# Kernel optimization log

Measured on AMD Instinct MI355X. Metric: run time of the kernel, lower is better.

The kernel has to match this reference:

```python
import jax, jax.numpy as jnp
import numpy as np

B = 512
V = 6890   # SMPL vertices
NJ = 24    # joints (global)
NB = 10    # shape betas
NP = 207   # pose blendshape features = 23*9
NJO = 19   # cocoplus output joints
PARENTS = np.array([0,0,0,0,1,2,3,4,5,6,7,8,9,9,9,12,13,14,16,17,18,19,20,21], dtype=np.int32)


def setup_inputs() -> dict:
    key = jax.random.key(0)
    ks = jax.random.split(key, 7)
    inputs = jax.random.normal(ks[0], (B, 82), jnp.float32) * 0.2  # [pose(72) | shape(10)]
    v_template = jax.random.normal(ks[1], (V, 3), jnp.float32)
    shapes = jax.random.normal(ks[2], (NB, V * 3), jnp.float32) * 0.01
    posedirs = jax.random.normal(ks[3], (NP, V * 3), jnp.float32) * 0.01
    jr = jax.random.uniform(ks[4], (V, NJ), jnp.float32)
    smpl_regressor = jr / jnp.sum(jr, axis=0, keepdims=True)          # columns sum to 1 over vertices
    w = jax.random.uniform(ks[5], (V, NJ), jnp.float32) ** 4
    lbs_weights = w / jnp.sum(w, axis=1, keepdims=True)               # rows sum to 1 over joints
    cr = jax.random.uniform(ks[6], (V, NJO), jnp.float32)
    joint_regressor = cr / jnp.sum(cr, axis=0, keepdims=True)
    parents = jnp.asarray(PARENTS)
    return {"inputs": inputs, "v_template": v_template, "shapes": shapes,
            "posedirs": posedirs, "smpl_regressor": smpl_regressor,
            "lbs_weights": lbs_weights, "joint_regressor": joint_regressor,
            "parents": parents}


def _rodrigues(pose):  # [B,72] -> [B,24,3,3]
    r = pose.reshape(-1, 3)
    angle = jnp.linalg.norm(r + 1e-8, axis=1, keepdims=True)  # [N,1]
    n = r / angle
    c = jnp.cos(angle)[:, :, None]   # [N,1,1]
    s = jnp.sin(angle)[:, :, None]
    outer = n[:, :, None] * n[:, None, :]
    z = jnp.zeros_like(n[:, 0])
    K = jnp.stack([z, -n[:, 2], n[:, 1],
                   n[:, 2], z, -n[:, 0],
                   -n[:, 1], n[:, 0], z], axis=1).reshape(-1, 3, 3)
    R = c * jnp.eye(3, dtype=pose.dtype) + (1.0 - c) * outer + s * K
    return R.reshape(-1, NJ, 3, 3)


def _make_A(R, t):  # R [B,3,3], t [B,3] -> [B,4,4]
    top = jnp.concatenate([R, t[:, :, None]], axis=2)
    bottom = jnp.broadcast_to(jnp.array([0., 0., 0., 1.], dtype=R.dtype), (R.shape[0], 1, 4))
    return jnp.concatenate([top, bottom], axis=1)


def _global_rigid(rotations, joints, parents_np):
    # sequential kinematic-chain composition over the fixed 24-joint tree
    res = [_make_A(rotations[:, 0], joints[:, 0])]
    for i in range(1, NJ):
        p = int(parents_np[i])
        t = joints[:, i] - joints[:, p]
        res.append(jnp.matmul(res[p], _make_A(rotations[:, i], t)))
    A_world = jnp.stack(res, axis=1)                 # [B,24,4,4]
    new_J = A_world[:, :, :3, 3]
    Jw0 = jnp.concatenate([joints, jnp.zeros(joints.shape[:2] + (1,), joints.dtype)], axis=2)[..., None]
    init_bone = jnp.matmul(A_world, Jw0)[..., 0]     # [B,24,4]
    pad = jnp.zeros_like(A_world).at[:, :, :, 3].set(init_bone)
    return new_J, A_world - pad


def reference(inputs, v_template, shapes, posedirs, smpl_regressor, lbs_weights, joint_regressor, parents):
    b = inputs.shape[0]
    pose = inputs[:, :72]
    beta = inputs[:, -10:]
    v_shaped = jnp.matmul(beta, shapes).reshape(b, V, 3) + v_template
    v_joints = jnp.einsum('bvc,vj->bjc', v_shaped, smpl_regressor)        # [B,24,3]
    rot = _rodrigues(pose)                                                # [B,24,3,3]
    pose_feature = (rot[:, 1:] - jnp.eye(3, dtype=rot.dtype)).reshape(b, -1)  # [B,207]
    v_posed = jnp.matmul(pose_feature, posedirs).reshape(b, V, 3) + v_shaped
    joint_transformed, A = _global_rigid(rot, v_joints, np.asarray(parents))
    T = jnp.einsum('vj,bjk->bvk', lbs_weights, A.reshape(b, NJ, 16)).reshape(b, V, 4, 4)
    v_homo = jnp.concatenate([v_posed, jnp.ones((b, V, 1), v_posed.dtype)], axis=2)
    vertices = jnp.einsum('bvij,bvj->bvi', T, v_homo)[:, :, :3]
    joints = jnp.einsum('bvc,vj->bjc', vertices, joint_regressor)         # [B,19,3]
    return vertices, joints, rot
```

## Files before the change

kernel.cpp:

```cpp
#include <hip/hip_runtime.h>

#define B_   512
#define V_   6890
#define V3_  20670
#define NJ_  24
#define NB_  10
#define NP_  207
#define NJO_ 19

typedef __attribute__((ext_vector_type(8))) short short8;
typedef __attribute__((ext_vector_type(8))) __bf16 bf16x8;
typedef __attribute__((ext_vector_type(4))) float f32x4;


#define SRB_   192
#define SRCH_  862
#define RODB_  48
#define TRB_   26

__global__ void __launch_bounds__(256) k_pre(const float* __restrict__ in,
                                             const float* __restrict__ shapes,
                                             const float* __restrict__ vt,
                                             const float* __restrict__ sreg,
                                             const float* __restrict__ jreg,
                                             float* __restrict__ srtr8,
                                             float* __restrict__ out_rot,
                                             float* __restrict__ pf_t,
                                             float* __restrict__ jreg_t,
                                             float* __restrict__ jout) {
  int blk = blockIdx.x;
  int tid = threadIdx.x;
  if (blk < SRB_) {
    int j  = blk >> 3;
    int ch = blk & 7;
    int vend = (ch + 1) * SRCH_; if (vend > V_) vend = V_;
    float acc[33];
#pragma unroll
    for (int a = 0; a < 33; a++) acc[a] = 0.f;
    for (int v = ch * SRCH_ + tid; v < vend; v += 256) {
      float w = sreg[v * NJ_ + j];
#pragma unroll
      for (int k = 0; k < NB_; k++) {
        const float* sp = shapes + k * V3_ + 3 * v;
#pragma unroll
        for (int c = 0; c < 3; c++) acc[k * 3 + c] += w * sp[c];
      }
#pragma unroll
      for (int c = 0; c < 3; c++) acc[30 + c] += w * vt[3 * v + c];
    }
    __shared__ float red[4][33];
    int wave = tid >> 6, lane = tid & 63;
#pragma unroll
    for (int a = 0; a < 33; a++) {
      float x = acc[a];
#pragma unroll
      for (int m = 1; m < 64; m <<= 1) x += __shfl_xor(x, m, 64);
      if (lane == 0) red[wave][a] = x;
    }
    __syncthreads();
    if (tid < 33) {
      float s = red[0][tid] + red[1][tid] + red[2][tid] + red[3][tid];
      float* dst = srtr8 + ch * 792;
      if (tid < 30) dst[((tid / 3) * NJ_ + j) * 3 + (tid % 3)] = s;
      else          dst[720 + j * 3 + (tid - 30)] = s;
    }
  } else if (blk < SRB_ + RODB_) {
    int idx = (blk - SRB_) * 256 + tid;
    int b = idx & (B_ - 1);
    int j = idx >> 9;
    const float* r = in + b * 82 + j * 3;
    float r0 = r[0], r1 = r[1], r2 = r[2];
    float ax = r0 + 1e-8f, ay = r1 + 1e-8f, az = r2 + 1e-8f;
    float angle = sqrtf(ax * ax + ay * ay + az * az);
    float inv = 1.0f / angle;
    float n0 = r0 * inv, n1 = r1 * inv, n2 = r2 * inv;
    float c = cosf(angle), s = sinf(angle);
    float ic = 1.0f - c;
    float R[9];
    R[0] = c + ic * n0 * n0;      R[1] = ic * n0 * n1 - s * n2;  R[2] = ic * n0 * n2 + s * n1;
    R[3] = ic * n1 * n0 + s * n2; R[4] = c + ic * n1 * n1;       R[5] = ic * n1 * n2 - s * n0;
    R[6] = ic * n2 * n0 - s * n1; R[7] = ic * n2 * n1 + s * n0;  R[8] = c + ic * n2 * n2;
    float* ro = out_rot + b * 216 + j * 9;
#pragma unroll
    for (int q = 0; q < 9; q++) ro[q] = R[q];
    if (j > 0) {
#pragma unroll
      for (int q = 0; q < 9; q++)
        pf_t[(size_t)((j - 1) * 9 + q) * B_ + b] = R[q] - ((q % 4 == 0) ? 1.0f : 0.0f);
    }
  } else {
    int idx = (blk - SRB_ - RODB_) * 256 + tid;
    for (int q = idx; q < B_ * NJO_ * 3; q += TRB_ * 256) jout[q] = 0.f;
    for (int e = idx; e < V_ * NJO_; e += TRB_ * 256) {
      int jo = e / V_;
      int v  = e - jo * V_;
      jreg_t[e] = jreg[v * NJO_ + jo];
    }
  }
}

__global__ void __launch_bounds__(192) k_chain(const float* __restrict__ in,
                                               const float* __restrict__ rot,
                                               const float* __restrict__ srtr8,
                                               const int* __restrict__ parents,
                                               float* __restrict__ Abuf) {
  (void)parents;
  constexpr int P[NJ_] = {0, 0, 0, 0, 1, 2, 3, 4, 5, 6, 7, 8, 9, 9, 9, 12, 13, 14,
                          16, 17, 18, 19, 20, 21};
  __shared__ float srl[792];
  int tid = threadIdx.x;
  for (int i = tid; i < 792; i += 192) {
    float s = 0.f;
#pragma unroll
    for (int ch = 0; ch < 8; ch++) s += srtr8[ch * 792 + i];
    srl[i] = s;
  }
  __syncthreads();
  int bl = tid & 63;
  int r  = tid >> 6;
  int b  = blockIdx.x * 64 + bl;
  float beta[NB_];
#pragma unroll
  for (int k = 0; k < NB_; k++) beta[k] = in[b * 82 + 72 + k];
  float J[NJ_][3];
#pragma unroll
  for (int j = 0; j < NJ_; j++) {
#pragma unroll
    for (int c = 0; c < 3; c++) {
      float s = srl[720 + j * 3 + c];
#pragma unroll
      for (int k = 0; k < NB_; k++) s += beta[k] * srl[(k * NJ_ + j) * 3 + c];
      J[j][c] = s;
    }
  }
  const float* Rb = rot + b * 216;
  float A[NJ_][4];
#pragma unroll
  for (int c = 0; c < 3; c++) A[0][c] = Rb[r * 3 + c];
  A[0][3] = J[0][r];
#pragma unroll
  for (int j = 1; j < NJ_; j++) {
    const int p = P[j];
    float t0 = J[j][0] - J[p][0];
    float t1 = J[j][1] - J[p][1];
    float t2 = J[j][2] - J[p][2];
    float Rj[9];
#pragma unroll
    for (int q = 0; q < 9; q++) Rj[q] = Rb[j * 9 + q];
    float p0 = A[p][0], p1 = A[p][1], p2 = A[p][2], p3 = A[p][3];
#pragma unroll
    for (int c = 0; c < 3; c++)
      A[j][c] = p0 * Rj[c] + p1 * Rj[3 + c] + p2 * Rj[6 + c];
    A[j][3] = p0 * t0 + p1 * t1 + p2 * t2 + p3;
  }
  float* Ab = Abuf + (size_t)b * 288 + r * 4;
#pragma unroll
  for (int j = 0; j < NJ_; j++) {
    float4 o;
    o.x = A[j][0]; o.y = A[j][1]; o.z = A[j][2];
    o.w = A[j][3] - (A[j][0] * J[j][0] + A[j][1] * J[j][1] + A[j][2] * J[j][2]);
    *reinterpret_cast<float4*>(Ab + j * 12) = o;
  }
}

#define PB_   8
#define BT_   32
#define GX_   108
#define GY_   16
#define NWG_  (GX_ * GY_)
#define NKT_  7
#define BUFS_ 6144
#define VPST_ 196

__device__ __forceinline__ unsigned f2bf(float x) {
  unsigned int u = __builtin_bit_cast(unsigned int, x);
  u += 0x7fffu + ((u >> 16) & 1u);
  return u >> 16;
}

__device__ __forceinline__ f32x4 mfma_bf16(short8 a, short8 b, f32x4 c) {
  return __builtin_amdgcn_mfma_f32_16x16x32_bf16(
      __builtin_bit_cast(bf16x8, a), __builtin_bit_cast(bf16x8, b), c, 0, 0, 0);
}

__global__ void __launch_bounds__(256) k_main(const float* __restrict__ in,
                                              const float* __restrict__ shapes,
                                              const float* __restrict__ vt,
                                              const float* __restrict__ posedirs,
                                              const float* __restrict__ lbs,
                                              const float* __restrict__ pf_t,
                                              const float* __restrict__ Abuf,
                                              float* __restrict__ verts) {
  __shared__ float smem[32 * VPST_];
  __shared__ float lbs_l[64 * 25];
  unsigned short* pds = reinterpret_cast<unsigned short*>(smem);

  int tid = threadIdx.x;
  int raw  = blockIdx.y * GX_ + blockIdx.x;
  int virt = (raw & 7) * (NWG_ / 8) + (raw >> 3);
  int vblk = virt >> 4;
  int bblk = virt & (GY_ - 1);
  int v0 = vblk * 64;
  int b0 = bblk * BT_;
  int nv = V_ - v0; if (nv > 64) nv = 64;
  for (int i = tid; i < nv * NJ_; i += 256)
    lbs_l[(i / NJ_) * 25 + (i % NJ_)] = lbs[(size_t)v0 * NJ_ + i];

  int lane = tid & 63;
  int g = tid >> 6;
  int v = v0 + lane;
  int vc = v < V_ ? v : V_ - 1;
  int ebase  = 3 * v0;
  int ebaseC = ebase; if (ebaseC > V3_ - 192) ebaseC = V3_ - 192;
  int lsh = ebase - ebaseC;

  int mt = g & 1;
  int nbase = (g >> 1) * 6;
  int bA = b0 + mt * 16 + (lane & 15);
  int kgrp = (lane >> 4) * 8;
  short8 afrag[NKT_];
#pragma unroll
  for (int kt = 0; kt < NKT_; kt++) {
    short8 a;
#pragma unroll
    for (int j = 0; j < 8; j++) {
      int rg = kt * 32 + kgrp + j;
      float fv = (rg < NP_) ? pf_t[(size_t)rg * B_ + bA] : 0.f;
      a[j] = (short)f2bf(fv);
    }
    afrag[kt] = a;
  }

  const int kg = g;

  {
    float sv[8][3];
#pragma unroll
    for (int kk = 0; kk < 8; kk++) {
      int rg = kg * 8 + kk; if (rg > NP_ - 1) rg = NP_ - 1;
      const float* src = posedirs + (size_t)rg * V3_ + ebaseC + lane;
      sv[kk][0] = src[0]; sv[kk][1] = src[64]; sv[kk][2] = src[128];
    }
    unsigned short* pw = pds;
#pragma unroll
    for (int j = 0; j < 3; j++) {
      uint4 w;
      w.x = f2bf(sv[0][j]) | (f2bf(sv[1][j]) << 16);
      w.y = f2bf(sv[2][j]) | (f2bf(sv[3][j]) << 16);
      w.z = f2bf(sv[4][j]) | (f2bf(sv[5][j]) << 16);
      w.w = f2bf(sv[6][j]) | (f2bf(sv[7][j]) << 16);
      *reinterpret_cast<uint4*>(pw + (kg * 192 + lane + j * 64) * 8) = w;
    }
  }
  __syncthreads();

  f32x4 acc[6];
#pragma unroll
  for (int n = 0; n < 6; n++) acc[n] = {0.f, 0.f, 0.f, 0.f};
  int ktlL = lane >> 4;
  int eLb  = (lane & 15);

  for (int c = 0; c < NKT_; c++) {
    float sv[8][3];
    const bool more = (c + 1 < NKT_);
    if (more) {
#pragma unroll
      for (int kk = 0; kk < 8; kk++) {
        int rg = (c + 1) * 32 + kg * 8 + kk; if (rg > NP_ - 1) rg = NP_ - 1;
        const float* src = posedirs + (size_t)rg * V3_ + ebaseC + lane;
        sv[kk][0] = src[0]; sv[kk][1] = src[64]; sv[kk][2] = src[128];
      }
    }
    const unsigned short* pr = pds + (c & 1) * BUFS_;
#pragma unroll
    for (int n = 0; n < 6; n++) {
      int eL = (nbase + n) * 16 + eLb;
      short8 bfrg = *reinterpret_cast<const short8*>(pr + (ktlL * 192 + eL) * 8);
      acc[n] = mfma_bf16(afrag[c], bfrg, acc[n]);
    }
    if (more) {
      unsigned short* pw = pds + ((c + 1) & 1) * BUFS_;
#pragma unroll
      for (int j = 0; j < 3; j++) {
        uint4 w;
        w.x = f2bf(sv[0][j]) | (f2bf(sv[1][j]) << 16);
        w.y = f2bf(sv[2][j]) | (f2bf(sv[3][j]) << 16);
        w.z = f2bf(sv[4][j]) | (f2bf(sv[5][j]) << 16);
        w.w = f2bf(sv[6][j]) | (f2bf(sv[7][j]) << 16);
        *reinterpret_cast<uint4*>(pw + (kg * 192 + lane + j * 64) * 8) = w;
      }
    }
    __syncthreads();
  }

#pragma unroll
  for (int n = 0; n < 6; n++) {
    int ecol = (nbase + n) * 16 + eLb;
#pragma unroll
    for (int reg = 0; reg < 4; reg++) {
      int brow = mt * 16 + (lane >> 4) * 4 + reg;
      smem[brow * VPST_ + ecol] = acc[n][reg];
    }
  }
  __syncthreads();

  int bb0 = __builtin_amdgcn_readfirstlane(b0 + g * PB_);
  int li = 3 * lane + lsh; if (v >= V_) li = 0;

  float acc2[PB_][3];
  {
    float t0 = vt[3 * vc + 0], t1 = vt[3 * vc + 1], t2 = vt[3 * vc + 2];
#pragma unroll
    for (int i = 0; i < PB_; i++) {
      int bl = g * PB_ + i;
      acc2[i][0] = t0 + smem[bl * VPST_ + li + 0];
      acc2[i][1] = t1 + smem[bl * VPST_ + li + 1];
      acc2[i][2] = t2 + smem[bl * VPST_ + li + 2];
    }
  }
#pragma unroll
  for (int k = 0; k < NB_; k++) {
    const float* sp = shapes + k * V3_ + 3 * vc;
    float s0 = sp[0], s1 = sp[1], s2 = sp[2];
#pragma unroll
    for (int i = 0; i < PB_; i++) {
      float bv = in[(size_t)(bb0 + i) * 82 + 72 + k];
      acc2[i][0] += bv * s0; acc2[i][1] += bv * s1; acc2[i][2] += bv * s2;
    }
  }
  float o[PB_][3];
#pragma unroll
  for (int i = 0; i < PB_; i++) { o[i][0] = 0.f; o[i][1] = 0.f; o[i][2] = 0.f; }
  for (int j = 0; j < NJ_; j++) {
    float w = lbs_l[lane * 25 + j];
#pragma unroll
    for (int i = 0; i < PB_; i++) {
      const float4* M4 = reinterpret_cast<const float4*>(Abuf + (size_t)(bb0 + i) * 288 + j * 12);
      float4 m0 = M4[0], m1 = M4[1], m2 = M4[2];
      float x = acc2[i][0], y = acc2[i][1], z = acc2[i][2];
      o[i][0] += w * (m0.x * x + m0.y * y + m0.z * z + m0.w);
      o[i][1] += w * (m1.x * x + m1.y * y + m1.z * z + m1.w);
      o[i][2] += w * (m2.x * x + m2.y * y + m2.z * z + m2.w);
    }
  }
  if (v < V_) {
#pragma unroll
    for (int i = 0; i < PB_; i++) {
      float* op = verts + (size_t)(bb0 + i) * (V_ * 3) + 3 * v;
      op[0] = o[i][0]; op[1] = o[i][1]; op[2] = o[i][2];
    }
  }
}

#define JCH_ 1728
__global__ void __launch_bounds__(256) k_joints(const float* __restrict__ verts,
                                                const float* __restrict__ jreg_t,
                                                float* __restrict__ jout) {
  int b = blockIdx.x;
  int ch = blockIdx.y;
  int tid = threadIdx.x;
  int vend = (ch + 1) * JCH_; if (vend > V_) vend = V_;
  float acc[NJO_ * 3];
#pragma unroll
  for (int a = 0; a < NJO_ * 3; a++) acc[a] = 0.f;
  const float* vb = verts + (size_t)b * V3_;
  for (int v2 = ch * JCH_ + 2 * tid; v2 < vend; v2 += 512) {
    const float2* p2 = reinterpret_cast<const float2*>(vb + 3 * v2);
    float2 a01 = p2[0], a23 = p2[1], a45 = p2[2];
    float x0 = a01.x, y0 = a01.y, z0 = a23.x;
    float x1 = a23.y, y1 = a45.x, z1 = a45.y;
#pragma unroll
    for (int jo = 0; jo < NJO_; jo++) {
      float2 w = *reinterpret_cast<const float2*>(jreg_t + (size_t)jo * V_ + v2);
      acc[jo * 3 + 0] += w.x * x0 + w.y * x1;
      acc[jo * 3 + 1] += w.x * y0 + w.y * y1;
      acc[jo * 3 + 2] += w.x * z0 + w.y * z1;
    }
  }
  __shared__ float red[4][NJO_ * 3];
  int wave = tid >> 6, lane = tid & 63;
#pragma unroll
  for (int a = 0; a < NJO_ * 3; a++) {
    float x = acc[a];
#pragma unroll
    for (int m = 1; m < 64; m <<= 1) x += __shfl_xor(x, m, 64);
    if (lane == 0) red[wave][a] = x;
  }
  __syncthreads();
  if (tid < NJO_ * 3) {
    float s = red[0][tid] + red[1][tid] + red[2][tid] + red[3][tid];
    atomicAdd(&jout[b * (NJO_ * 3) + tid], s);
  }
}

extern "C" void kernel_launch(void* const* d_in, const int* in_sizes, int n_in,
                              void* d_out, int out_size, void* d_ws, size_t ws_size,
                              hipStream_t stream) {
  const float* inputs   = (const float*)d_in[0];
  const float* v_templ  = (const float*)d_in[1];
  const float* shapes   = (const float*)d_in[2];
  const float* posedirs = (const float*)d_in[3];
  const float* sreg     = (const float*)d_in[4];
  const float* lbs      = (const float*)d_in[5];
  const float* jreg     = (const float*)d_in[6];
  const int*   parents  = (const int*)d_in[7];

  float* out   = (float*)d_out;
  float* verts = out;
  float* jout  = out + 10583040;
  float* rot   = out + 10612224;

  float* ws     = (float*)d_ws;
  float* pf_t   = ws;
  float* Abuf   = ws + 105984;
  float* srtr8  = ws + 105984 + 147456;
  float* jreg_t = srtr8 + 6336;

  k_pre  <<<SRB_ + RODB_ + TRB_, 256, 0, stream>>>(inputs, shapes, v_templ, sreg, jreg,
                                                   srtr8, rot, pf_t, jreg_t, jout);
  k_chain<<<8, 192, 0, stream>>>(inputs, rot, srtr8, parents, Abuf);
  dim3 gmain(GX_, GY_);
  k_main <<<gmain, 256, 0, stream>>>(inputs, shapes, v_templ, posedirs, lbs, pf_t, Abuf, verts);
  dim3 gj(B_, 4);
  k_joints<<<gj, 256, 0, stream>>>(verts, jreg_t, jout);
}
```

Baseline: 264.8 us.

## Single-buffer posedirs LDS tile, store pose offsets as bf16, stage rotations in LDS

k_main drops the double-buffered posedirs LDS tile for a single buffer with an extra barrier, and stores the GEMM result tile as bf16 instead of fp32. Together these shrink shared memory per block and may allow more resident workgroups. The cost is an extra synchronisation per k-step and bf16 rounding of the pose-corrective offsets. k_chain now stages each block's rotation matrices into padded LDS before the sequential chain, replacing strided global reads.

```diff
diff --git a/kernel.cpp b/kernel.cpp
--- a/kernel.cpp
+++ b/kernel.cpp
@@ -108,17 +108,23 @@
   constexpr int P[NJ_] = {0, 0, 0, 0, 1, 2, 3, 4, 5, 6, 7, 8, 9, 9, 9, 12, 13, 14,
                           16, 17, 18, 19, 20, 21};
   __shared__ float srl[792];
+  __shared__ float rot_l[64 * 217];
   int tid = threadIdx.x;
+  int b0blk = blockIdx.x * 64;
   for (int i = tid; i < 792; i += 192) {
     float s = 0.f;
 #pragma unroll
     for (int ch = 0; ch < 8; ch++) s += srtr8[ch * 792 + i];
     srl[i] = s;
+  }
+  for (int idx = tid; idx < 64 * 216; idx += 192) {
+    int bl = idx / 216, q = idx - bl * 216;
+    rot_l[bl * 217 + q] = rot[(size_t)(b0blk + bl) * 216 + q];
   }
   __syncthreads();
   int bl = tid & 63;
   int r  = tid >> 6;
-  int b  = blockIdx.x * 64 + bl;
+  int b  = b0blk + bl;
   float beta[NB_];
 #pragma unroll
   for (int k = 0; k < NB_; k++) beta[k] = in[b * 82 + 72 + k];
@@ -133,7 +139,7 @@
       J[j][c] = s;
     }
   }
-  const float* Rb = rot + b * 216;
+  const float* Rb = rot_l + bl * 217;
   float A[NJ_][4];
 #pragma unroll
   for (int c = 0; c < 3; c++) A[0][c] = Rb[r * 3 + c];
@@ -169,13 +175,16 @@
 #define GY_   16
 #define NWG_  (GX_ * GY_)
 #define NKT_  7
-#define BUFS_ 6144
-#define VPST_ 196
+#define VPSTB_ 200
 
 __device__ __forceinline__ unsigned f2bf(float x) {
   unsigned int u = __builtin_bit_cast(unsigned int, x);
   u += 0x7fffu + ((u >> 16) & 1u);
   return u >> 16;
+}
+__device__ __forceinline__ float bf2f(unsigned short h) {
+  unsigned int u = ((unsigned int)h) << 16;
+  return __builtin_bit_cast(float, u);
 }
 
 __device__ __forceinline__ f32x4 mfma_bf16(short8 a, short8 b, f32x4 c) {
@@ -191,9 +200,9 @@
                                               const float* __restrict__ pf_t,
                                               const float* __restrict__ Abuf,
                                               float* __restrict__ verts) {
-  __shared__ float smem[32 * VPST_];
+  __shared__ unsigned short smem_s[32 * VPSTB_];
   __shared__ float lbs_l[64 * 25];
-  unsigned short* pds = reinterpret_cast<unsigned short*>(smem);
+  unsigned short* pds = smem_s;
 
   int tid = threadIdx.x;
   int raw  = blockIdx.y * GX_ + blockIdx.x;
@@ -241,7 +250,6 @@
       const float* src = posedirs + (size_t)rg * V3_ + ebaseC + lane;
       sv[kk][0] = src[0]; sv[kk][1] = src[64]; sv[kk][2] = src[128];
     }
-    unsigned short* pw = pds;
 #pragma unroll
     for (int j = 0; j < 3; j++) {
       uint4 w;
@@ -249,7 +257,7 @@
       w.y = f2bf(sv[2][j]) | (f2bf(sv[3][j]) << 16);
       w.z = f2bf(sv[4][j]) | (f2bf(sv[5][j]) << 16);
       w.w = f2bf(sv[6][j]) | (f2bf(sv[7][j]) << 16);
-      *reinterpret_cast<uint4*>(pw + (kg * 192 + lane + j * 64) * 8) = w;
+      *reinterpret_cast<uint4*>(pds + (kg * 192 + lane + j * 64) * 8) = w;
     }
   }
   __syncthreads();
@@ -271,15 +279,14 @@
         sv[kk][0] = src[0]; sv[kk][1] = src[64]; sv[kk][2] = src[128];
       }
     }
-    const unsigned short* pr = pds + (c & 1) * BUFS_;
 #pragma unroll
     for (int n = 0; n < 6; n++) {
       int eL = (nbase + n) * 16 + eLb;
-      short8 bfrg = *reinterpret_cast<const short8*>(pr + (ktlL * 192 + eL) * 8);
+      short8 bfrg = *reinterpret_cast<const short8*>(pds + (ktlL * 192 + eL) * 8);
       acc[n] = mfma_bf16(afrag[c], bfrg, acc[n]);
     }
+    __syncthreads();
     if (more) {
-      unsigned short* pw = pds + ((c + 1) & 1) * BUFS_;
 #pragma unroll
       for (int j = 0; j < 3; j++) {
         uint4 w;
@@ -287,10 +294,10 @@
         w.y = f2bf(sv[2][j]) | (f2bf(sv[3][j]) << 16);
         w.z = f2bf(sv[4][j]) | (f2bf(sv[5][j]) << 16);
         w.w = f2bf(sv[6][j]) | (f2bf(sv[7][j]) << 16);
-        *reinterpret_cast<uint4*>(pw + (kg * 192 + lane + j * 64) * 8) = w;
+        *reinterpret_cast<uint4*>(pds + (kg * 192 + lane + j * 64) * 8) = w;
       }
-    }
-    __syncthreads();
+      __syncthreads();
+    }
   }
 
 #pragma unroll
@@ -299,7 +306,7 @@
 #pragma unroll
     for (int reg = 0; reg < 4; reg++) {
       int brow = mt * 16 + (lane >> 4) * 4 + reg;
-      smem[brow * VPST_ + ecol] = acc[n][reg];
+      smem_s[brow * VPSTB_ + ecol] = (unsigned short)f2bf(acc[n][reg]);
     }
   }
   __syncthreads();
@@ -313,9 +320,9 @@
 #pragma unroll
     for (int i = 0; i < PB_; i++) {
       int bl = g * PB_ + i;
-      acc2[i][0] = t0 + smem[bl * VPST_ + li + 0];
-      acc2[i][1] = t1 + smem[bl * VPST_ + li + 1];
-      acc2[i][2] = t2 + smem[bl * VPST_ + li + 2];
+      acc2[i][0] = t0 + bf2f(smem_s[bl * VPSTB_ + li + 0]);
+      acc2[i][1] = t1 + bf2f(smem_s[bl * VPSTB_ + li + 1]);
+      acc2[i][2] = t2 + bf2f(smem_s[bl * VPSTB_ + li + 2]);
     }
   }
 #pragma unroll
```

After: 283.6 us. 1.07x slower.
